# Kernel optimization log

Hardware: AMD Instinct MI355X
Metric: run time of the kernel (lower is better)

Reference implementation:

```python
import jax, jax.numpy as jnp
import numpy as np

B, N, D, H = 8, 1024, 1024, 16
DH = D // H
SCALE = DH ** -0.5
NEG = -1e9


def setup_inputs() -> dict:
    key = jax.random.key(0)
    k1, k2, k3, k4 = jax.random.split(key, 4)
    x = jax.random.normal(k1, (B, N, D), dtype=jnp.float32)
    mask = jax.random.randint(k2, (B, N), 0, 2, dtype=jnp.int32)
    w_qkv = jax.random.normal(k3, (D, 3 * D), dtype=jnp.float32) * (D ** -0.5)
    w_out = jax.random.normal(k4, (D, D), dtype=jnp.float32) * (D ** -0.5)
    b_out = jnp.zeros((D,), dtype=jnp.float32)
    return {"x": x, "mask": mask, "w_qkv": w_qkv, "w_out": w_out, "b_out": b_out}


def reference(x, mask, w_qkv, w_out, b_out):
    b, n, d = x.shape
    qkv = x @ w_qkv  # [b, n, 3d]
    q, k, v = jnp.split(qkv, 3, axis=-1)
    # [b, n, d] -> [b, h, n, dh]
    reshape = lambda t: t.reshape(b, n, H, DH).transpose(0, 2, 1, 3)
    q, k, v = reshape(q), reshape(k), reshape(v)
    dots = jnp.einsum("bhqd,bhkd->bhqk", q, k) * SCALE  # [b, h, n, n]
    # mask [b, n] -> [b, 1, n]; broadcasts over heads and query dim (masks keys)
    m = (mask == 0)[:, None, None, :]
    dots = jnp.where(m, NEG, dots)
    attn = jax.nn.softmax(dots, axis=-1)
    out = jnp.einsum("bhqk,bhkd->bhqd", attn, v)  # [b, h, n, dh]
    out = out.transpose(0, 2, 1, 3).reshape(b, n, d)  # [b, n, d]
    out = out @ w_out + b_out
    return out, attn
```

## Files before the change

kernel.cpp:

```cpp
#include <hip/hip_runtime.h>
#include <hip/hip_bf16.h>

typedef unsigned short u16;
typedef __attribute__((ext_vector_type(8))) short bf16x8;
typedef __attribute__((ext_vector_type(4))) float f32x4;

#define DEVI __device__ __forceinline__

constexpr float SCALE = 0.125f;

DEVI float bf2f(u16 u) { unsigned v = ((unsigned)u) << 16; float f; __builtin_memcpy(&f, &v, 4); return f; }
DEVI u16 f2bf(float f) { __hip_bfloat16 h = __float2bfloat16(f); u16 u; __builtin_memcpy(&u, &h, 2); return u; }

DEVI void gload_lds16(const u16* g, u16* l) {
    __builtin_amdgcn_global_load_lds(
        (const __attribute__((address_space(1))) unsigned int*)g,
        (__attribute__((address_space(3))) unsigned int*)l, 16, 0, 0);
}

__global__ __launch_bounds__(256) void cast_f32_bf16(const float* __restrict__ in,
                                                     u16* __restrict__ out, int n) {
    int i = (blockIdx.x * 256 + threadIdx.x) * 4;
    if (i >= n) return;
    float4 v = *(const float4*)(in + i);
    ushort4 o;
    o.x = f2bf(v.x); o.y = f2bf(v.y); o.z = f2bf(v.z); o.w = f2bf(v.w);
    *(ushort4*)(out + i) = o;
}

__global__ __launch_bounds__(256) void transpose_f32_bf16(const float* __restrict__ in,
                                                          u16* __restrict__ out,
                                                          int R, int C) {
    __shared__ u16 t[64][65];
    int r0 = blockIdx.y * 64, c0 = blockIdx.x * 64;
    int tid = threadIdx.x;
    for (int i = 0; i < 16; i++) {
        int idx = tid + i * 256; int r = idx >> 6, c = idx & 63;
        t[r][c] = f2bf(in[(size_t)(r0 + r) * C + c0 + c]);
    }
    __syncthreads();
    for (int i = 0; i < 16; i++) {
        int idx = tid + i * 256; int c = idx >> 6, r = idx & 63;
        out[(size_t)(c0 + c) * R + r0 + r] = t[r][c];
    }
}

__global__ __launch_bounds__(256) void make_vt(const u16* __restrict__ qkv,
                                               u16* __restrict__ vt) {
    __shared__ u16 t[64][65];
    int bh = blockIdx.y; int b = bh >> 4, h = bh & 15;
    int n0 = blockIdx.x * 64;
    int tid = threadIdx.x;
    const u16* src = qkv + (size_t)b * 1024 * 3072 + 2048 + h * 64;
    for (int i = 0; i < 16; i++) {
        int idx = tid + i * 256; int n = idx >> 6, d = idx & 63;
        t[n][d] = src[(size_t)(n0 + n) * 3072 + d];
    }
    __syncthreads();
    u16* dst = vt + (size_t)bh * 64 * 1024;
    for (int i = 0; i < 16; i++) {
        int idx = tid + i * 256; int d = idx >> 6, n = idx & 63;
        dst[(size_t)d * 1024 + n0 + n] = t[n][d];
    }
}

template <bool BIAS, bool F32OUT>
__global__ __launch_bounds__(256) void gemm_bt(const u16* __restrict__ A,
                                               const u16* __restrict__ Bt,
                                               const float* __restrict__ bias,
                                               void* __restrict__ Cv,
                                               int M, int N, int K) {
    __shared__ alignas(16) u16 As[128 * 64];
    __shared__ alignas(16) u16 Bs[128 * 64];
    int tid = threadIdx.x;
    int wave = tid >> 6, lane = tid & 63, quad = lane >> 4, lm = lane & 15;
    int bm = blockIdx.y * 128, bn = blockIdx.x * 128;
    int wm = (wave >> 1) * 64, wn = (wave & 1) * 64;

    f32x4 acc[4][4];
    for (int i = 0; i < 4; i++) for (int j = 0; j < 4; j++) acc[i][j] = f32x4{0.f, 0.f, 0.f, 0.f};

    int lrow8 = lane >> 3;
    int lcol  = (lane & 7) * 8;

    for (int kb = 0; kb < K; kb += 64) {
        for (int i = 0; i < 4; i++) {
            int c = wave * 4 + i;
            int row = c * 8 + lrow8;
            gload_lds16(A  + (size_t)(bm + row) * K + kb + lcol, &As[c * 512 + lane * 8]);
            gload_lds16(Bt + (size_t)(bn + row) * K + kb + lcol, &Bs[c * 512 + lane * 8]);
        }
        __syncthreads();
        for (int ks = 0; ks < 2; ks++) {
            bf16x8 af[4], bfr[4];
            for (int mt = 0; mt < 4; mt++)
                af[mt] = *(const bf16x8*)(&As[(wm + mt * 16 + lm) * 64 + ks * 32 + quad * 8]);
            for (int nt = 0; nt < 4; nt++)
                bfr[nt] = *(const bf16x8*)(&Bs[(wn + nt * 16 + lm) * 64 + ks * 32 + quad * 8]);
            for (int mt = 0; mt < 4; mt++)
                for (int nt = 0; nt < 4; nt++)
                    acc[mt][nt] = __builtin_amdgcn_mfma_f32_16x16x32_bf16(
                        af[mt], bfr[nt], acc[mt][nt], 0, 0, 0);
        }
        __syncthreads();
    }
    for (int mt = 0; mt < 4; mt++)
        for (int nt = 0; nt < 4; nt++) {
            int col = bn + wn + nt * 16 + lm;
            float bv = BIAS ? bias[col] : 0.f;
            for (int r = 0; r < 4; r++) {
                int row = bm + wm + mt * 16 + quad * 4 + r;
                if (F32OUT) ((float*)Cv)[(size_t)row * N + col] = acc[mt][nt][r] + bv;
                else        ((u16*)Cv)[(size_t)row * N + col] = f2bf(acc[mt][nt][r] + bv);
            }
        }
}

__global__ __launch_bounds__(256) void attn_mfma(const u16* __restrict__ qkv,
                                                 const u16* __restrict__ vt,
                                                 const int* __restrict__ mask,
                                                 float* __restrict__ attn_out,
                                                 u16* __restrict__ o_ws) {
    __shared__ alignas(16) u16 Ks[64 * 64];
    __shared__ alignas(16) u16 Vs[64 * 64];
    constexpr int LDP = 72;
    __shared__ alignas(16) u16 Ps[64 * LDP];

    int tid = threadIdx.x;
    int wave = tid >> 6, lane = tid & 63, quad = lane >> 4, lm = lane & 15;

    int flat = blockIdx.y * gridDim.x + blockIdx.x;
    int swz = (flat & 7) * 256 + (flat >> 3);
    int bh = swz >> 4, qb = swz & 15;
    int b = bh >> 4, h = bh & 15;
    int qrow0 = qb * 64 + wave * 16;

    int srow = lane >> 3;
    int scol = (lane & 7) * 8;

    bf16x8 qf[2];
    {
        const u16* qptr = qkv + (size_t)(b * 1024 + qrow0 + lm) * 3072 + h * 64 + quad * 8;
        qf[0] = *(const bf16x8*)(qptr);
        qf[1] = *(const bf16x8*)(qptr + 32);
    }
    const u16* kbase  = qkv + (size_t)b * 1024 * 3072 + 1024 + h * 64;
    const u16* vtbase = vt + (size_t)bh * 64 * 1024;
    const int* mrow   = mask + b * 1024;

    float l_r[4] = {0.f, 0.f, 0.f, 0.f};
    for (int kb = 0; kb < 16; kb++) {
        for (int i = 0; i < 2; i++) {
            int c = wave * 2 + i;
            gload_lds16(kbase + (size_t)(kb * 64 + c * 8 + srow) * 3072 + scol,
                        &Ks[c * 512 + lane * 8]);
        }
        __syncthreads();
        f32x4 acc[4];
        for (int nt = 0; nt < 4; nt++) acc[nt] = f32x4{0.f, 0.f, 0.f, 0.f};
        for (int ks = 0; ks < 2; ks++)
            for (int nt = 0; nt < 4; nt++) {
                bf16x8 kf = *(const bf16x8*)(&Ks[(nt * 16 + lm) * 64 + ks * 32 + quad * 8]);
                acc[nt] = __builtin_amdgcn_mfma_f32_16x16x32_bf16(qf[ks], kf, acc[nt], 0, 0, 0);
            }
        for (int nt = 0; nt < 4; nt++) {
            bool mk = (mrow[kb * 64 + nt * 16 + lm] != 0);
            for (int r = 0; r < 4; r++)
                l_r[r] += mk ? __expf(acc[nt][r] * SCALE) : 0.f;
        }
        __syncthreads();
    }
    float invl[4];
    for (int r = 0; r < 4; r++) {
        float l = l_r[r];
        for (int s = 8; s >= 1; s >>= 1) l += __shfl_xor(l, s, 64);
        invl[r] = 1.0f / l;
    }

    f32x4 oacc[4];
    for (int nt = 0; nt < 4; nt++) oacc[nt] = f32x4{0.f, 0.f, 0.f, 0.f};
    for (int kb = 0; kb < 16; kb++) {
        for (int i = 0; i < 2; i++) {
            int c = wave * 2 + i;
            gload_lds16(kbase + (size_t)(kb * 64 + c * 8 + srow) * 3072 + scol,
                        &Ks[c * 512 + lane * 8]);
            gload_lds16(vtbase + (size_t)(c * 8 + srow) * 1024 + kb * 64 + scol,
                        &Vs[c * 512 + lane * 8]);
        }
        __syncthreads();
        f32x4 acc[4];
        for (int nt = 0; nt < 4; nt++) acc[nt] = f32x4{0.f, 0.f, 0.f, 0.f};
        for (int ks = 0; ks < 2; ks++)
            for (int nt = 0; nt < 4; nt++) {
                bf16x8 kf = *(const bf16x8*)(&Ks[(nt * 16 + lm) * 64 + ks * 32 + quad * 8]);
                acc[nt] = __builtin_amdgcn_mfma_f32_16x16x32_bf16(qf[ks], kf, acc[nt], 0, 0, 0);
            }
        for (int nt = 0; nt < 4; nt++) {
            bool mk = (mrow[kb * 64 + nt * 16 + lm] != 0);
            for (int r = 0; r < 4; r++) {
                float p = mk ? __expf(acc[nt][r] * SCALE) * invl[r] : 0.f;
                attn_out[((size_t)bh * 1024 + qb * 64 + wave * 16 + quad * 4 + r) * 1024
                         + kb * 64 + nt * 16 + lm] = p;
                Ps[(wave * 16 + quad * 4 + r) * LDP + nt * 16 + lm] = f2bf(p);
            }
        }
        for (int ks = 0; ks < 2; ks++) {
            bf16x8 pf = *(const bf16x8*)(&Ps[(wave * 16 + lm) * LDP + ks * 32 + quad * 8]);
            for (int nt = 0; nt < 4; nt++) {
                bf16x8 vf = *(const bf16x8*)(&Vs[(nt * 16 + lm) * 64 + ks * 32 + quad * 8]);
                oacc[nt] = __builtin_amdgcn_mfma_f32_16x16x32_bf16(pf, vf, oacc[nt], 0, 0, 0);
            }
        }
        __syncthreads();
    }
    for (int nt = 0; nt < 4; nt++)
        for (int r = 0; r < 4; r++) {
            int row = qb * 64 + wave * 16 + quad * 4 + r;
            o_ws[(size_t)(b * 1024 + row) * 1024 + h * 64 + nt * 16 + lm] = f2bf(oacc[nt][r]);
        }
}

extern "C" void kernel_launch(void* const* d_in, const int* in_sizes, int n_in,
                              void* d_out, int out_size, void* d_ws, size_t ws_size,
                              hipStream_t stream) {
    const float* x    = (const float*)d_in[0];
    const int*   mask = (const int*)d_in[1];
    const float* wqkv = (const float*)d_in[2];
    const float* wout = (const float*)d_in[3];
    const float* bout = (const float*)d_in[4];

    float* out  = (float*)d_out;
    float* attn = out + (size_t)8192 * 1024;

    char* ws = (char*)d_ws;
    u16* xbf   = (u16*)(ws);
    u16* vt    = xbf;
    u16* qkv   = (u16*)(ws + 16777216);
    u16* o_ws  = (u16*)(ws + 67108864);
    u16* wqkvT = (u16*)(ws + 83886080);
    u16* woutT = (u16*)(ws + 90177536);

    cast_f32_bf16<<<dim3(8192), 256, 0, stream>>>(x, xbf, 8388608);
    transpose_f32_bf16<<<dim3(48, 16), 256, 0, stream>>>(wqkv, wqkvT, 1024, 3072);
    transpose_f32_bf16<<<dim3(16, 16), 256, 0, stream>>>(wout, woutT, 1024, 1024);
    gemm_bt<false, false><<<dim3(24, 64), 256, 0, stream>>>(xbf, wqkvT, nullptr, qkv, 8192, 3072, 1024);
    make_vt<<<dim3(16, 128), 256, 0, stream>>>(qkv, vt);
    attn_mfma<<<dim3(16, 128), 256, 0, stream>>>(qkv, vt, mask, attn, o_ws);
    gemm_bt<true, true><<<dim3(8, 64), 256, 0, stream>>>(o_ws, woutT, bout, out, 8192, 1024, 1024);
}
```

Baseline: 835.0 us.

## Double-buffer K/V LDS tiles and XOR-swizzle LDS layout in attention kernel

```diff
diff --git a/kernel.cpp b/kernel.cpp
--- a/kernel.cpp
+++ b/kernel.cpp
@@ -121,8 +121,8 @@
                                                  const int* __restrict__ mask,
                                                  float* __restrict__ attn_out,
                                                  u16* __restrict__ o_ws) {
-    __shared__ alignas(16) u16 Ks[64 * 64];
-    __shared__ alignas(16) u16 Vs[64 * 64];
+    __shared__ alignas(16) u16 Ks[2 * 64 * 64];
+    __shared__ alignas(16) u16 Vs[2 * 64 * 64];
     constexpr int LDP = 72;
     __shared__ alignas(16) u16 Ps[64 * LDP];
 
@@ -136,7 +136,16 @@
     int qrow0 = qb * 64 + wave * 16;
 
     int srow = lane >> 3;
-    int scol = (lane & 7) * 8;
+    int scol = (((lane & 7) ^ srow) << 3);
+
+    const u16* kbase  = qkv + (size_t)b * 1024 * 3072 + 1024 + h * 64;
+    const u16* vtbase = vt + (size_t)bh * 64 * 1024;
+    const int* mrow   = mask + b * 1024;
+
+    for (int i = 0; i < 2; i++) {
+        int c = wave * 2 + i;
+        gload_lds16(kbase + (size_t)(c * 8 + srow) * 3072 + scol, &Ks[c * 512 + lane * 8]);
+    }
 
     bf16x8 qf[2];
     {
@@ -144,31 +153,37 @@
         qf[0] = *(const bf16x8*)(qptr);
         qf[1] = *(const bf16x8*)(qptr + 32);
     }
-    const u16* kbase  = qkv + (size_t)b * 1024 * 3072 + 1024 + h * 64;
-    const u16* vtbase = vt + (size_t)bh * 64 * 1024;
-    const int* mrow   = mask + b * 1024;
+
+    int fsw0 = ((0 * 4 + quad) ^ (lm & 7)) << 3;
+    int fsw1 = ((1 * 4 + quad) ^ (lm & 7)) << 3;
 
     float l_r[4] = {0.f, 0.f, 0.f, 0.f};
+    int cur = 0;
     for (int kb = 0; kb < 16; kb++) {
-        for (int i = 0; i < 2; i++) {
-            int c = wave * 2 + i;
-            gload_lds16(kbase + (size_t)(kb * 64 + c * 8 + srow) * 3072 + scol,
-                        &Ks[c * 512 + lane * 8]);
-        }
-        __syncthreads();
+        __syncthreads();
+        if (kb < 15) {
+            int nb = (cur ^ 1) * 4096;
+            for (int i = 0; i < 2; i++) {
+                int c = wave * 2 + i;
+                gload_lds16(kbase + (size_t)((kb + 1) * 64 + c * 8 + srow) * 3072 + scol,
+                            &Ks[nb + c * 512 + lane * 8]);
+            }
+        }
+        const u16* K0 = &Ks[cur * 4096];
         f32x4 acc[4];
         for (int nt = 0; nt < 4; nt++) acc[nt] = f32x4{0.f, 0.f, 0.f, 0.f};
-        for (int ks = 0; ks < 2; ks++)
-            for (int nt = 0; nt < 4; nt++) {
-                bf16x8 kf = *(const bf16x8*)(&Ks[(nt * 16 + lm) * 64 + ks * 32 + quad * 8]);
-                acc[nt] = __builtin_amdgcn_mfma_f32_16x16x32_bf16(qf[ks], kf, acc[nt], 0, 0, 0);
-            }
+        for (int nt = 0; nt < 4; nt++) {
+            bf16x8 kf0 = *(const bf16x8*)(&K0[(nt * 16 + lm) * 64 + fsw0]);
+            bf16x8 kf1 = *(const bf16x8*)(&K0[(nt * 16 + lm) * 64 + fsw1]);
+            acc[nt] = __builtin_amdgcn_mfma_f32_16x16x32_bf16(qf[0], kf0, acc[nt], 0, 0, 0);
+            acc[nt] = __builtin_amdgcn_mfma_f32_16x16x32_bf16(qf[1], kf1, acc[nt], 0, 0, 0);
+        }
         for (int nt = 0; nt < 4; nt++) {
             bool mk = (mrow[kb * 64 + nt * 16 + lm] != 0);
             for (int r = 0; r < 4; r++)
                 l_r[r] += mk ? __expf(acc[nt][r] * SCALE) : 0.f;
         }
-        __syncthreads();
+        cur ^= 1;
     }
     float invl[4];
     for (int r = 0; r < 4; r++) {
@@ -177,24 +192,37 @@
         invl[r] = 1.0f / l;
     }
 
+    for (int i = 0; i < 2; i++) {
+        int c = wave * 2 + i;
+        gload_lds16(kbase + (size_t)(c * 8 + srow) * 3072 + scol, &Ks[c * 512 + lane * 8]);
+        gload_lds16(vtbase + (size_t)(c * 8 + srow) * 1024 + scol, &Vs[c * 512 + lane * 8]);
+    }
+
     f32x4 oacc[4];
     for (int nt = 0; nt < 4; nt++) oacc[nt] = f32x4{0.f, 0.f, 0.f, 0.f};
+    cur = 0;
     for (int kb = 0; kb < 16; kb++) {
-        for (int i = 0; i < 2; i++) {
-            int c = wave * 2 + i;
-            gload_lds16(kbase + (size_t)(kb * 64 + c * 8 + srow) * 3072 + scol,
-                        &Ks[c * 512 + lane * 8]);
-            gload_lds16(vtbase + (size_t)(c * 8 + srow) * 1024 + kb * 64 + scol,
-                        &Vs[c * 512 + lane * 8]);
-        }
-        __syncthreads();
+        __syncthreads();
+        if (kb < 15) {
+            int nb = (cur ^ 1) * 4096;
+            for (int i = 0; i < 2; i++) {
+                int c = wave * 2 + i;
+                gload_lds16(kbase + (size_t)((kb + 1) * 64 + c * 8 + srow) * 3072 + scol,
+                            &Ks[nb + c * 512 + lane * 8]);
+                gload_lds16(vtbase + (size_t)(c * 8 + srow) * 1024 + (kb + 1) * 64 + scol,
+                            &Vs[nb + c * 512 + lane * 8]);
+            }
+        }
+        const u16* K0 = &Ks[cur * 4096];
+        const u16* V0 = &Vs[cur * 4096];
         f32x4 acc[4];
         for (int nt = 0; nt < 4; nt++) acc[nt] = f32x4{0.f, 0.f, 0.f, 0.f};
-        for (int ks = 0; ks < 2; ks++)
-            for (int nt = 0; nt < 4; nt++) {
-                bf16x8 kf = *(const bf16x8*)(&Ks[(nt * 16 + lm) * 64 + ks * 32 + quad * 8]);
-                acc[nt] = __builtin_amdgcn_mfma_f32_16x16x32_bf16(qf[ks], kf, acc[nt], 0, 0, 0);
-            }
+        for (int nt = 0; nt < 4; nt++) {
+            bf16x8 kf0 = *(const bf16x8*)(&K0[(nt * 16 + lm) * 64 + fsw0]);
+            bf16x8 kf1 = *(const bf16x8*)(&K0[(nt * 16 + lm) * 64 + fsw1]);
+            acc[nt] = __builtin_amdgcn_mfma_f32_16x16x32_bf16(qf[0], kf0, acc[nt], 0, 0, 0);
+            acc[nt] = __builtin_amdgcn_mfma_f32_16x16x32_bf16(qf[1], kf1, acc[nt], 0, 0, 0);
+        }
         for (int nt = 0; nt < 4; nt++) {
             bool mk = (mrow[kb * 64 + nt * 16 + lm] != 0);
             for (int r = 0; r < 4; r++) {
@@ -206,12 +234,13 @@
         }
         for (int ks = 0; ks < 2; ks++) {
             bf16x8 pf = *(const bf16x8*)(&Ps[(wave * 16 + lm) * LDP + ks * 32 + quad * 8]);
+            int fsw = (ks == 0) ? fsw0 : fsw1;
             for (int nt = 0; nt < 4; nt++) {
-                bf16x8 vf = *(const bf16x8*)(&Vs[(nt * 16 + lm) * 64 + ks * 32 + quad * 8]);
+                bf16x8 vf = *(const bf16x8*)(&V0[(nt * 16 + lm) * 64 + fsw]);
                 oacc[nt] = __builtin_amdgcn_mfma_f32_16x16x32_bf16(pf, vf, oacc[nt], 0, 0, 0);
             }
         }
-        __syncthreads();
+        cur ^= 1;
     }
     for (int nt = 0; nt < 4; nt++)
         for (int r = 0; r < 4; r++) {
```

Result: no change. 836.9 us (+0.2%).
